# Performance work log

Hardware: AMD Instinct MI355X
Metric: run time of the kernel (lower is better)

Reference implementation:

```python
import jax, jax.numpy as jnp
import numpy as np

N_TRAJ = 64   # num_trajectory
T_STEP = 64   # t_step
D_FEAT = 256
EPS = 1e-8    # torch F.cosine_similarity eps


def setup_inputs() -> dict:
    key = jax.random.key(0)
    k1, k2 = jax.random.split(key)
    z = jax.random.normal(k1, (2 * N_TRAJ * T_STEP, D_FEAT), dtype=jnp.float32)
    done = jax.random.randint(k2, (N_TRAJ, T_STEP), 0, 2).astype(jnp.int32)
    return {"z": z, "done": done}


def reference(z, done):
    N, T = N_TRAJ, T_STEP
    NT = N * T
    M = 2 * NT  # z.shape[0]

    # --- replicate the sequential done-rewrite loop, vectorized ---
    # After the torch loop: done[r, j] == 1 iff (some original done strictly
    # before j in row r) AND original done[r, j] == 0.
    done_f = done.astype(jnp.float32)
    prior = jnp.concatenate(
        [jnp.zeros((N, 1), jnp.float32),
         jax.lax.cummax(done_f, axis=1)[:, :-1]], axis=1)  # exclusive prefix-OR
    done_final = prior * (1.0 - done_f)
    dv = (1.0 - done_final).reshape(-1)  # done_mask vector, [NT]

    # block_diag(N blocks of ones(T,T)).repeat(2,2) == trajectory-id equality on tiled ids
    traj = jnp.arange(NT) // T            # [NT]
    traj2 = jnp.tile(traj, 2)             # [2NT]
    tm = (traj2[:, None] == traj2[None, :]).astype(jnp.float32)  # temporal_mask, [M,M]

    dv2 = jnp.tile(dv, 2)                 # repeat(2,2) of outer product == outer of tiled vec
    dm = dv2[:, None] * dv2[None, :] * tm  # done_mask, [M,M]

    eye = jnp.eye(M, dtype=jnp.float32)
    positive_mask = (1.0 - dm) * (1.0 - tm) + eye  # values in {0,1}

    # all-pairs cosine similarity (norms clamped at eps, as in torch)
    zn = z / jnp.maximum(jnp.linalg.norm(z, axis=-1, keepdims=True), EPS)
    logits = zn @ zn.T  # [M, M]

    pos_w = 1.0 - positive_mask        # entries selected by nonzero(1 - positive_mask)
    neg_w = positive_mask - eye        # entries selected by nonzero(positive_mask - eye)
    positive_sim = jnp.sum(logits * pos_w) / jnp.sum(pos_w)
    negative_sim = jnp.sum(logits * neg_w) / jnp.sum(neg_w)
    return positive_sim, negative_sim
```

## Files before the change

kernel.cpp:

```cpp
#include <hip/hip_runtime.h>

#define NTRAJ 64
#define TSTEP 64
#define DFEAT 256
#define NT    (NTRAJ * TSTEP)
#define MROWS (2 * NT)

#define POS_DEN 1040384.0
#define NEG_DEN 66060288.0

__global__ __launch_bounds__(256)
void tsl_group_kernel(const float* __restrict__ z,
                      float* __restrict__ St,
                      float* __restrict__ diag)
{
    const int g    = blockIdx.x;
    const int tid  = threadIdx.x;
    const int w    = tid >> 6;
    const int lane = tid & 63;

    float a0 = 0.f, a1 = 0.f, a2 = 0.f, a3 = 0.f;
    float dpart = 0.f;

    #pragma unroll 4
    for (int r = 0; r < 32; ++r) {
        const int m   = w * 32 + r;
        const int row = (m < 64) ? (g * 64 + m) : (NT + g * 64 + (m - 64));
        const float4 v = *reinterpret_cast<const float4*>(
            z + (size_t)row * DFEAT + (size_t)lane * 4);

        float ss = v.x * v.x + v.y * v.y + v.z * v.z + v.w * v.w;
        #pragma unroll
        for (int off = 32; off > 0; off >>= 1)
            ss += __shfl_xor(ss, off, 64);

        const float rinv = 1.0f / fmaxf(sqrtf(ss), 1e-8f);
        a0 += v.x * rinv;
        a1 += v.y * rinv;
        a2 += v.z * rinv;
        a3 += v.w * rinv;
        if (lane == 0) dpart += ss * rinv * rinv;
    }

    __shared__ float4 S4[4][64];
    __shared__ float dd[4];
    S4[w][lane] = make_float4(a0, a1, a2, a3);
    if (lane == 0) dd[w] = dpart;
    __syncthreads();

    const float* Sf = reinterpret_cast<const float*>(S4);
    const float s = Sf[0 * 256 + tid] + Sf[1 * 256 + tid] +
                    Sf[2 * 256 + tid] + Sf[3 * 256 + tid];
    St[g * 256 + tid] = s;
    if (tid == 0) diag[g] = dd[0] + dd[1] + dd[2] + dd[3];
}

__global__ __launch_bounds__(256)
void tsl_final_kernel(const float* __restrict__ St,
                      const float* __restrict__ diag,
                      float* __restrict__ out)
{
    const int tid = threadIdx.x;

    double g1 = 0.0, col = 0.0;
    #pragma unroll 8
    for (int g = 0; g < 64; ++g) {
        const float v = St[g * 256 + tid];
        g1  += (double)v * (double)v;
        col += (double)v;
    }
    const double g2 = col * col;
    const double dg = (tid < 64) ? (double)diag[tid] : 0.0;

    __shared__ double r1[256], r2[256], r3[256];
    r1[tid] = g1; r2[tid] = g2; r3[tid] = dg;
    __syncthreads();
    #pragma unroll
    for (int s = 128; s > 0; s >>= 1) {
        if (tid < s) {
            r1[tid] += r1[tid + s];
            r2[tid] += r2[tid + s];
            r3[tid] += r3[tid + s];
        }
        __syncthreads();
    }

    if (tid == 0) {
        const double G1 = r1[0], G2 = r2[0], DG = r3[0];
        out[0] = (float)((G1 - DG) / POS_DEN);
        out[1] = (float)((G2 - G1) / NEG_DEN);
    }
}

extern "C" void kernel_launch(void* const* d_in, const int* in_sizes, int n_in,
                              void* d_out, int out_size, void* d_ws, size_t ws_size,
                              hipStream_t stream) {
    const float* z = (const float*)d_in[0];
    float* St   = (float*)d_ws;
    float* diag = (float*)((char*)d_ws + 64 * 256 * sizeof(float));
    float* out  = (float*)d_out;

    tsl_group_kernel<<<64, 256, 0, stream>>>(z, St, diag);
    tsl_final_kernel<<<1, 256, 0, stream>>>(St, diag, out);
}
```

Baseline: 16.79 us.

## Split row normalization across 256 blocks and use shuffle reduction in final kernel

The first kernel now launches 256 blocks of 512 threads. Each block handles 32 contiguous rows, four per wavefront, instead of 64 blocks each looping over 128 rows. This spreads the memory-bound load of z across more CUs and lowers per-thread serial latency. The final kernel now combines four partial sums per trajectory group, with the pairing chosen to match the trajectory tiling. It also swaps the LDS tree reduction for wave shuffles plus a small shared array. In exchange, the partial buffer is larger and the single-block final kernel reads four times as much data.

Result: faster. 15.93 us (-5.1%).

```diff
diff --git a/kernel.cpp b/kernel.cpp
--- a/kernel.cpp
+++ b/kernel.cpp
@@ -9,12 +9,13 @@
 #define POS_DEN 1040384.0
 #define NEG_DEN 66060288.0
 
-__global__ __launch_bounds__(256)
-void tsl_group_kernel(const float* __restrict__ z,
-                      float* __restrict__ St,
-                      float* __restrict__ diag)
+
+__global__ __launch_bounds__(512)
+void tsl_partial_kernel(const float* __restrict__ z,
+                        float* __restrict__ P,
+                        float* __restrict__ Dp)
 {
-    const int g    = blockIdx.x;
+    const int b    = blockIdx.x;
     const int tid  = threadIdx.x;
     const int w    = tid >> 6;
     const int lane = tid & 63;
@@ -22,10 +23,9 @@
     float a0 = 0.f, a1 = 0.f, a2 = 0.f, a3 = 0.f;
     float dpart = 0.f;
 
-    #pragma unroll 4
-    for (int r = 0; r < 32; ++r) {
-        const int m   = w * 32 + r;
-        const int row = (m < 64) ? (g * 64 + m) : (NT + g * 64 + (m - 64));
+    #pragma unroll
+    for (int r = 0; r < 4; ++r) {
+        const int row = b * 32 + w * 4 + r;
         const float4 v = *reinterpret_cast<const float4*>(
             z + (size_t)row * DFEAT + (size_t)lane * 4);
 
@@ -42,51 +42,60 @@
         if (lane == 0) dpart += ss * rinv * rinv;
     }
 
-    __shared__ float4 S4[4][64];
-    __shared__ float dd[4];
-    S4[w][lane] = make_float4(a0, a1, a2, a3);
+    __shared__ float S[8][256];
+    __shared__ float dd[8];
+    *reinterpret_cast<float4*>(&S[w][lane * 4]) = make_float4(a0, a1, a2, a3);
     if (lane == 0) dd[w] = dpart;
     __syncthreads();
 
-    const float* Sf = reinterpret_cast<const float*>(S4);
-    const float s = Sf[0 * 256 + tid] + Sf[1 * 256 + tid] +
-                    Sf[2 * 256 + tid] + Sf[3 * 256 + tid];
-    St[g * 256 + tid] = s;
-    if (tid == 0) diag[g] = dd[0] + dd[1] + dd[2] + dd[3];
+    if (tid < 256) {
+        float s = 0.f;
+        #pragma unroll
+        for (int k = 0; k < 8; ++k) s += S[k][tid];
+        P[b * 256 + tid] = s;
+        if (tid == 0) {
+            float d = 0.f;
+            #pragma unroll
+            for (int k = 0; k < 8; ++k) d += dd[k];
+            Dp[b] = d;
+        }
+    }
 }
 
 __global__ __launch_bounds__(256)
-void tsl_final_kernel(const float* __restrict__ St,
-                      const float* __restrict__ diag,
+void tsl_final_kernel(const float* __restrict__ P,
+                      const float* __restrict__ Dp,
                       float* __restrict__ out)
 {
-    const int tid = threadIdx.x;
+    const int tid  = threadIdx.x;
+    const int w    = tid >> 6;
+    const int lane = tid & 63;
 
     double g1 = 0.0, col = 0.0;
     #pragma unroll 8
     for (int g = 0; g < 64; ++g) {
-        const float v = St[g * 256 + tid];
-        g1  += (double)v * (double)v;
-        col += (double)v;
+        const float s = P[(2 * g) * 256 + tid] + P[(2 * g + 1) * 256 + tid] +
+                        P[(128 + 2 * g) * 256 + tid] + P[(129 + 2 * g) * 256 + tid];
+        g1  += (double)s * (double)s;
+        col += (double)s;
     }
-    const double g2 = col * col;
-    const double dg = (tid < 64) ? (double)diag[tid] : 0.0;
+    double g2 = col * col;
+    double dg = (double)Dp[tid];
 
-    __shared__ double r1[256], r2[256], r3[256];
-    r1[tid] = g1; r2[tid] = g2; r3[tid] = dg;
+    #pragma unroll
+    for (int off = 32; off > 0; off >>= 1) {
+        g1 += __shfl_down(g1, off, 64);
+        g2 += __shfl_down(g2, off, 64);
+        dg += __shfl_down(dg, off, 64);
+    }
+    __shared__ double W[3][4];
+    if (lane == 0) { W[0][w] = g1; W[1][w] = g2; W[2][w] = dg; }
     __syncthreads();
-    #pragma unroll
-    for (int s = 128; s > 0; s >>= 1) {
-        if (tid < s) {
-            r1[tid] += r1[tid + s];
-            r2[tid] += r2[tid + s];
-            r3[tid] += r3[tid + s];
-        }
-        __syncthreads();
-    }
 
     if (tid == 0) {
-        const double G1 = r1[0], G2 = r2[0], DG = r3[0];
+        const double G1 = W[0][0] + W[0][1] + W[0][2] + W[0][3];
+        const double G2 = W[1][0] + W[1][1] + W[1][2] + W[1][3];
+        const double DG = W[2][0] + W[2][1] + W[2][2] + W[2][3];
         out[0] = (float)((G1 - DG) / POS_DEN);
         out[1] = (float)((G2 - G1) / NEG_DEN);
     }
@@ -96,10 +105,10 @@
                               void* d_out, int out_size, void* d_ws, size_t ws_size,
                               hipStream_t stream) {
     const float* z = (const float*)d_in[0];
-    float* St   = (float*)d_ws;
-    float* diag = (float*)((char*)d_ws + 64 * 256 * sizeof(float));
-    float* out  = (float*)d_out;
+    float* P   = (float*)d_ws;
+    float* Dp  = (float*)((char*)d_ws + 256 * 256 * sizeof(float));
+    float* out = (float*)d_out;
 
-    tsl_group_kernel<<<64, 256, 0, stream>>>(z, St, diag);
-    tsl_final_kernel<<<1, 256, 0, stream>>>(St, diag, out);
+    tsl_partial_kernel<<<256, 512, 0, stream>>>(z, P, Dp);
+    tsl_final_kernel<<<1, 256, 0, stream>>>(P, Dp, out);
 }
```
